# Kernel tuning notes

Hardware: AMD Instinct MI355X
Metric: run time of the kernel (lower is better)

## Reference

```python
import jax, jax.numpy as jnp
import numpy as np

B, T, C, H, KV, D = 2, 2048, 1024, 16, 4, 64
VE_GATE_CH = 32


def _rope(x, cos, sin):
    # x: (B,T,h,D); cos/sin: (1,T,1,D//2); half-split rotary
    d = x.shape[-1] // 2
    x1, x2 = x[..., :d], x[..., d:]
    return jnp.concatenate([x1 * cos + x2 * sin, -x1 * sin + x2 * cos], axis=-1)


def _rms_norm(x, eps=1.1920929e-07):
    # F.rms_norm with no weight; eps defaults to finfo(fp32).eps
    return x * jax.lax.rsqrt(jnp.mean(x * x, axis=-1, keepdims=True) + eps)


def setup_inputs() -> dict:
    key = jax.random.key(0)
    ks = jax.random.split(key, 8)
    x = jax.random.normal(ks[0], (B, T, C), dtype=jnp.float32)
    ve = jax.random.normal(ks[1], (B, T, KV * D), dtype=jnp.float32)
    # standard RoPE tables, half-dim = D//2
    inv_freq = 1.0 / (10000.0 ** (np.arange(0, D, 2, dtype=np.float32) / D))  # (32,)
    freqs = np.arange(T, dtype=np.float32)[:, None] * inv_freq[None, :]       # (T,32)
    cos = jnp.asarray(np.cos(freqs))[None, :, None, :]
    sin = jnp.asarray(np.sin(freqs))[None, :, None, :]
    s = 0.02
    Wq = jax.random.normal(ks[2], (C, H * D), dtype=jnp.float32) * s
    Wk = jax.random.normal(ks[3], (C, KV * D), dtype=jnp.float32) * s
    Wv = jax.random.normal(ks[4], (C, KV * D), dtype=jnp.float32) * s
    Wo = jax.random.normal(ks[5], (C, C), dtype=jnp.float32) * s
    Wg = jax.random.normal(ks[6], (VE_GATE_CH, KV), dtype=jnp.float32) * s
    return {"x": x, "ve": ve, "cos": cos, "sin": sin,
            "Wq": Wq, "Wk": Wk, "Wv": Wv, "Wo": Wo, "Wg": Wg,
            "window": 1024}


def reference(x, ve, cos, sin, Wq, Wk, Wv, Wo, Wg, window):
    b, t, c = x.shape
    q = (x @ Wq).reshape(b, t, H, D)
    k = (x @ Wk).reshape(b, t, KV, D)
    v = (x @ Wv).reshape(b, t, KV, D)
    # value-embedding gating: gate = 2*sigmoid(x[..., :32] @ Wg)
    gate = 2.0 * jax.nn.sigmoid(x[..., :VE_GATE_CH] @ Wg)  # (B,T,KV)
    v = v + gate[..., None] * ve.reshape(b, t, KV, D)
    q = _rms_norm(_rope(q, cos, sin))
    k = _rms_norm(_rope(k, cos, sin))
    # GQA: repeat_interleave kv heads to match query heads
    groups = H // KV
    k = jnp.repeat(k, groups, axis=2)  # (B,T,H,D)
    v = jnp.repeat(v, groups, axis=2)
    scale = 1.0 / jnp.sqrt(jnp.asarray(D, dtype=q.dtype))
    scores = jnp.einsum("bthd,bshd->bhts", q, k) * scale  # (B,H,T,T)
    rows = jnp.arange(t)[:, None]
    cols = jnp.arange(t)[None, :]
    mask = (cols <= rows) & (cols > rows - window)  # causal sliding window
    scores = jnp.where(mask[None, None], scores, jnp.finfo(scores.dtype).min)
    attn = jax.nn.softmax(scores, axis=-1)
    y = jnp.einsum("bhts,bshd->bthd", attn, v).reshape(b, t, c)
    return y @ Wo
```

## Files before the change

### kernel.cpp

```cpp
#include <hip/hip_runtime.h>
#include <hip/hip_bf16.h>

#define B_ 2
#define T_ 2048
#define C_ 1024
#define H_ 16
#define KV_ 4
#define D_ 64
#define M_ (B_*T_)

typedef __attribute__((ext_vector_type(4))) float f32x4;
typedef __attribute__((ext_vector_type(8))) short bf16x8;

__device__ __forceinline__ float exp2fast(float x) {
  return __builtin_amdgcn_exp2f(x);
}

__device__ __forceinline__ unsigned short f2bfu(float f) {
  unsigned u = __builtin_bit_cast(unsigned, f);
  u += 0x7FFFu + ((u >> 16) & 1u);
  return (unsigned short)(u >> 16);
}

__device__ __forceinline__ short f2bf(float f) {
  return (short)f2bfu(f);
}

__device__ __forceinline__ float bf2f(short s) {
  unsigned u = ((unsigned)(unsigned short)s) << 16;
  return __builtin_bit_cast(float, u);
}

__device__ __forceinline__ unsigned cvtpk(float a, float b) {
  unsigned r;
  asm("v_cvt_pk_bf16_f32 %0, %1, %2" : "=v"(r) : "v"(a), "v"(b));
  return r;
}

__device__ __forceinline__ void gld_lds16(const void* g, void* l) {
  __builtin_amdgcn_global_load_lds(
      (const __attribute__((address_space(1))) void*)g,
      (__attribute__((address_space(3))) void*)l, 16, 0, 0);
}

__global__ __launch_bounds__(256) void k_prep(const float* __restrict__ xin,
                                              short* __restrict__ xb,
                                              const float* __restrict__ Wq,
                                              const float* __restrict__ Wk,
                                              const float* __restrict__ Wv,
                                              const float* __restrict__ Wo,
                                              short* __restrict__ wT,
                                              short* __restrict__ woT) {
  __shared__ float tile[32][33];
  const int bid = blockIdx.x;
  const int tid = threadIdx.x;
  if (bid < 4096) {
    int i = (bid * 256 + tid) * 4;
    float4 f = *(const float4*)(xin + i);
    short4 s;
    s.x = f2bf(f.x); s.y = f2bf(f.y); s.z = f2bf(f.z); s.w = f2bf(f.w);
    *(short4*)(xb + i) = s;
    return;
  }
  const int tb = bid - 4096;
  const int bx = tb % 80;
  const int by = tb / 80;
  const int tx = tid & 31, ty = tid >> 5;
  const float* in; short* out; int Ncol, cb;
  if (bx < 32)      { in = Wq; out = wT;                       Ncol = 1024; cb = bx; }
  else if (bx < 40) { in = Wk; out = wT + (size_t)1024 * 1024; Ncol = 256;  cb = bx - 32; }
  else if (bx < 48) { in = Wv; out = wT + (size_t)1280 * 1024; Ncol = 256;  cb = bx - 40; }
  else              { in = Wo; out = woT;                      Ncol = 1024; cb = bx - 48; }
  const int R = 1024;
  int c0 = cb * 32, r0 = by * 32;
#pragma unroll
  for (int i = 0; i < 32; i += 8)
    tile[ty + i][tx] = in[(size_t)(r0 + ty + i) * Ncol + c0 + tx];
  __syncthreads();
#pragma unroll
  for (int i = 0; i < 32; i += 8)
    out[(size_t)(c0 + ty + i) * R + r0 + tx] = f2bf(tile[tx][ty + i]);
}

__global__ __launch_bounds__(256) void k_gemm64(const short* __restrict__ A,
                                                const short* __restrict__ Bt,
                                                float* __restrict__ C,
                                                int M, int N, int K) {
  __shared__ short sA[64 * 64];
  __shared__ short sB[128 * 64];
  const int tid = threadIdx.x;
  const int wid = tid >> 6, lane = tid & 63;
  const int g = lane >> 4, c = lane & 15;
  const int wm = wid >> 1, wn = wid & 1;
  const int m0 = blockIdx.y * 64, n0 = blockIdx.x * 128;
  const int strow = tid >> 3;
  const int scol  = ((tid & 7) ^ (strow & 7)) * 8;
  const int sw = c & 7;

  const short* Ag = A + (size_t)(m0 + strow) * K + scol;
  const short* Bg = Bt + (size_t)(n0 + strow) * K + scol;
  const int ldbase = wid * 512;

  f32x4 acc[2][4] = {};

  for (int k0 = 0; k0 < K; k0 += 64) {
#pragma unroll
    for (int i = 0; i < 2; ++i)
      gld_lds16(Ag + (size_t)(i * 32) * K + k0, &sA[i * 2048 + ldbase]);
#pragma unroll
    for (int i = 0; i < 4; ++i)
      gld_lds16(Bg + (size_t)(i * 32) * K + k0, &sB[i * 2048 + ldbase]);
    __syncthreads();
#pragma unroll
    for (int kk = 0; kk < 2; ++kk) {
      bf16x8 af[2], bfr[4];
#pragma unroll
      for (int i = 0; i < 2; ++i)
        af[i] = *(const bf16x8*)&sA[(wm * 32 + i * 16 + c) * 64 + ((kk * 4 + g) ^ sw) * 8];
#pragma unroll
      for (int j = 0; j < 4; ++j)
        bfr[j] = *(const bf16x8*)&sB[(wn * 64 + j * 16 + c) * 64 + ((kk * 4 + g) ^ sw) * 8];
#pragma unroll
      for (int i = 0; i < 2; ++i)
#pragma unroll
        for (int j = 0; j < 4; ++j)
          acc[i][j] = __builtin_amdgcn_mfma_f32_16x16x32_bf16(af[i], bfr[j], acc[i][j], 0, 0, 0);
    }
    __syncthreads();
  }
#pragma unroll
  for (int i = 0; i < 2; ++i)
#pragma unroll
    for (int j = 0; j < 4; ++j) {
      int row = m0 + wm * 32 + i * 16 + g * 4;
      int col = n0 + wn * 64 + j * 16 + c;
      float* cp = C + (size_t)row * N + col;
#pragma unroll
      for (int r = 0; r < 4; ++r) cp[(size_t)r * N] = acc[i][j][r];
    }
}

__global__ __launch_bounds__(256) void k_gemm_qkv(const short* __restrict__ A,
                                                  const short* __restrict__ Bt,
                                                  short* __restrict__ qkvb,
                                                  short* __restrict__ qb,
                                                  short* __restrict__ kbb,
                                                  const float* __restrict__ cosp,
                                                  const float* __restrict__ sinp) {
  __shared__ short sA[64 * 64];
  __shared__ short sB[128 * 64];
  const int N = 1536, K = 1024;
  const int tid = threadIdx.x;
  const int wid = tid >> 6, lane = tid & 63;
  const int g = lane >> 4, c = lane & 15;
  const int wm = wid >> 1, wn = wid & 1;
  const int m0 = blockIdx.y * 64, n0 = blockIdx.x * 128;
  const int strow = tid >> 3;
  const int scol  = ((tid & 7) ^ (strow & 7)) * 8;
  const int sw = c & 7;

  const short* Ag = A + (size_t)(m0 + strow) * K + scol;
  const short* Bg = Bt + (size_t)(n0 + strow) * K + scol;
  const int ldbase = wid * 512;

  f32x4 acc[2][4] = {};

  for (int k0 = 0; k0 < K; k0 += 64) {
#pragma unroll
    for (int i = 0; i < 2; ++i)
      gld_lds16(Ag + (size_t)(i * 32) * K + k0, &sA[i * 2048 + ldbase]);
#pragma unroll
    for (int i = 0; i < 4; ++i)
      gld_lds16(Bg + (size_t)(i * 32) * K + k0, &sB[i * 2048 + ldbase]);
    __syncthreads();
#pragma unroll
    for (int kk = 0; kk < 2; ++kk) {
      bf16x8 af[2], bfr[4];
#pragma unroll
      for (int i = 0; i < 2; ++i)
        af[i] = *(const bf16x8*)&sA[(wm * 32 + i * 16 + c) * 64 + ((kk * 4 + g) ^ sw) * 8];
#pragma unroll
      for (int j = 0; j < 4; ++j)
        bfr[j] = *(const bf16x8*)&sB[(wn * 64 + j * 16 + c) * 64 + ((kk * 4 + g) ^ sw) * 8];
#pragma unroll
      for (int i = 0; i < 2; ++i)
#pragma unroll
        for (int j = 0; j < 4; ++j)
          acc[i][j] = __builtin_amdgcn_mfma_f32_16x16x32_bf16(af[i], bfr[j], acc[i][j], 0, 0, 0);
    }
    __syncthreads();
  }

  const int head = blockIdx.x * 2 + wn;
  const int b = m0 >> 11;
  const int tbase = (m0 & (T_ - 1)) + wm * 32;
  if (head < 20) {
    short* outbase = (head < 16)
        ? qb  + ((size_t)(b * H_ + head) * T_) * D_
        : kbb + ((size_t)(b * KV_ + (head - 16)) * T_) * D_;
#pragma unroll
    for (int i = 0; i < 2; ++i)
#pragma unroll
      for (int r = 0; r < 4; ++r) {
        const int t = tbase + i * 16 + g * 4 + r;
        const float ca = cosp[t * 32 + c],      sa = sinp[t * 32 + c];
        const float cbv = cosp[t * 32 + 16 + c], sbv = sinp[t * 32 + 16 + c];
        const float f0 = acc[i][0][r], f1 = acc[i][1][r];
        const float f2 = acc[i][2][r], f3 = acc[i][3][r];
        const float r0 = f0 * ca + f2 * sa;
        const float r1 = f1 * cbv + f3 * sbv;
        const float r2 = f2 * ca - f0 * sa;
        const float r3 = f3 * cbv - f1 * sbv;
        float ss = (r0 * r0 + r1 * r1) + (r2 * r2 + r3 * r3);
        ss += __shfl_xor(ss, 1);
        ss += __shfl_xor(ss, 2);
        ss += __shfl_xor(ss, 4);
        ss += __shfl_xor(ss, 8);
        const float sc = rsqrtf(ss * (1.0f / 64.0f) + 1.1920929e-07f);
        unsigned w0 = cvtpk(r0 * sc, r1 * sc);
        unsigned w1 = cvtpk(r2 * sc, r3 * sc);
        unsigned long long w = ((unsigned long long)w1 << 32) | w0;
        *(unsigned long long*)(outbase + (size_t)t * D_ + c * 4) = w;
      }
  } else {
#pragma unroll
    for (int i = 0; i < 2; ++i)
#pragma unroll
      for (int j = 0; j < 4; ++j) {
        int row = m0 + wm * 32 + i * 16 + g * 4;
        int col = n0 + wn * 64 + j * 16 + c;
        short* cp = qkvb + (size_t)row * N + col;
#pragma unroll
        for (int r = 0; r < 4; ++r) cp[(size_t)r * N] = f2bf(acc[i][j][r]);
      }
  }
}

__global__ __launch_bounds__(256) void k_vtrans(const short* __restrict__ qkvb,
                                                const float* __restrict__ ve,
                                                const float* __restrict__ x,
                                                const float* __restrict__ Wg,
                                                short* __restrict__ vT) {
  const int t0 = blockIdx.x * 64;
  const int bk = blockIdx.y;
  const int b = bk >> 2, kv = bk & 3;
  const int tx = threadIdx.x;
  const int ty = threadIdx.y;
  __shared__ float tile[64][65];
  __shared__ float sgate[64];
  if (ty == 0) {
    const int row = b * T_ + t0 + tx;
    const float* xr = x + (size_t)row * C_;
    float a = 0.0f;
#pragma unroll 8
    for (int kk = 0; kk < 32; ++kk) a = fmaf(xr[kk], Wg[kk * KV_ + kv], a);
    sgate[tx] = 2.0f / (1.0f + __expf(-a));
  }
  __syncthreads();
#pragma unroll
  for (int i = 0; i < 16; ++i) {
    const int tr = ty + 4 * i;
    const int row = b * T_ + t0 + tr;
    float gt = sgate[tr];
    float v = bf2f(qkvb[(size_t)row * 1536 + 1280 + kv * 64 + tx]);
    v = fmaf(gt, ve[(size_t)row * (KV_ * D_) + kv * 64 + tx], v);
    tile[tr][tx] = v;
  }
  __syncthreads();
#pragma unroll
  for (int i = 0; i < 16; ++i) {
    const int d = ty + 4 * i;
    vT[((size_t)bk * 64 + d) * T_ + t0 + tx] = f2bf(tile[tx][d]);
  }
}

__global__ __launch_bounds__(512, 6) void k_attn(const short* __restrict__ qg,
                                                 const short* __restrict__ kg,
                                                 const short* __restrict__ vg,
                                                 short* __restrict__ yb,
                                                 const int* __restrict__ winp) {
  const int wsz = *winp;
  const int qt = blockIdx.x, bh = blockIdx.y;
  const int b = bh >> 4, h = bh & 15;
  const int kvh = h >> 2;
  const int tid = threadIdx.x;
  const int wid = tid >> 6, lane = tid & 63;
  const int g = lane >> 4, c = lane & 15;
  const int t0 = qt * 128 + wid * 16;

  __shared__ short sK[2][64 * 64];
  __shared__ short sV[2][64 * 64];
  __shared__ short spt_all[8][16][72];
  short (*spt)[72] = spt_all[wid];

  const short* qbase = qg + ((size_t)(b * H_ + h) * T_ + t0) * D_;
  const bf16x8 bq0 = *(const bf16x8*)(qbase + c * D_ + g * 8);
  const bf16x8 bq1 = *(const bf16x8*)(qbase + c * D_ + 32 + g * 8);
  const short* kbase = kg + (size_t)(b * KV_ + kvh) * T_ * D_;
  const short* vbase = vg + (size_t)(b * KV_ + kvh) * D_ * T_;

  const int srow0 = tid >> 3;
  const int sq    = ((tid & 7) ^ (srow0 & 7)) * 8;
  const int ldst0 = wid * 512;

  float m = -20000.0f, l = 0.0f;
  f32x4 o[4] = {};

  int lo = t0 - wsz + 1; if (lo < 0) lo = 0;
  const int kt_lo_w = lo >> 6;
  const int kt_hi_w = (t0 + 15) >> 6;
  int lou = qt * 128 - wsz + 1; if (lou < 0) lou = 0;
  const int kt_lo_u = lou >> 6;
  const int kt_hi_u = 2 * qt + 1;
  const int qgl = t0 + c;
  const float SC2 = 0.125f * 1.44269504088896340736f;

  {
    const short* ksrc = kbase + (size_t)(kt_lo_u * 64 + srow0) * D_ + sq;
    gld_lds16(ksrc, &sK[0][ldst0]);
    const short* vsrc = vbase + (size_t)srow0 * T_ + kt_lo_u * 64 + sq;
    gld_lds16(vsrc, &sV[0][ldst0]);
  }
  __syncthreads();

  int cb = 0;
  for (int kt = kt_lo_u; kt <= kt_hi_u; ++kt) {
    const int kc0 = kt * 64;
    if (kt < kt_hi_u) {
      const short* ksrc = kbase + (size_t)((kt + 1) * 64 + srow0) * D_ + sq;
      gld_lds16(ksrc, &sK[cb ^ 1][ldst0]);
      const short* vsrc = vbase + (size_t)srow0 * T_ + (kt + 1) * 64 + sq;
      gld_lds16(vsrc, &sV[cb ^ 1][ldst0]);
    }
    if (kt >= kt_lo_w && kt <= kt_hi_w) {
      f32x4 s[4] = {};
#pragma unroll
      for (int cj = 0; cj < 4; ++cj) {
        const int rbase = (cj * 16 + c) * 64;
        const int sw = (c & 7);
        bf16x8 k0 = *(const bf16x8*)&sK[cb][rbase + ((g ^ sw) * 8)];
        bf16x8 k1 = *(const bf16x8*)&sK[cb][rbase + (((4 + g) ^ sw) * 8)];
        s[cj] = __builtin_amdgcn_mfma_f32_16x16x32_bf16(k0, bq0, s[cj], 0, 0, 0);
        s[cj] = __builtin_amdgcn_mfma_f32_16x16x32_bf16(k1, bq1, s[cj], 0, 0, 0);
      }
      const bool edge = (kt >= kt_hi_w) || (kt <= kt_lo_w + 1);
      float tmax = -3.0e38f;
#pragma unroll
      for (int cj = 0; cj < 4; ++cj)
#pragma unroll
        for (int r = 0; r < 4; ++r) {
          float v = s[cj][r];
          if (edge) {
            int kv = kc0 + cj * 16 + 4 * g + r;
            v = (kv <= qgl && kv > qgl - wsz) ? v : -1.0e9f;
            s[cj][r] = v;
          }
          tmax = fmaxf(tmax, v);
        }
      tmax = fmaxf(tmax, __shfl_xor(tmax, 16));
      tmax = fmaxf(tmax, __shfl_xor(tmax, 32));
      const float tms = tmax * SC2;
      if (!__all(tms <= m + 8.0f)) {
        const float nm = fmaxf(m, tms);
        const float fr = exp2fast(m - nm);
        m = nm;
        l *= fr;
#pragma unroll
        for (int nd = 0; nd < 4; ++nd)
#pragma unroll
          for (int r = 0; r < 4; ++r) o[nd][r] *= fr;
      }
      const float negm = -m;
      float psum = 0.0f;
      unsigned pb[8];
#pragma unroll
      for (int cj = 0; cj < 4; ++cj) {
        float p0 = exp2fast(fmaf(s[cj][0], SC2, negm));
        float p1 = exp2fast(fmaf(s[cj][1], SC2, negm));
        float p2 = exp2fast(fmaf(s[cj][2], SC2, negm));
        float p3 = exp2fast(fmaf(s[cj][3], SC2, negm));
        psum += (p0 + p1) + (p2 + p3);
        pb[2 * cj]     = cvtpk(p0, p1);
        pb[2 * cj + 1] = cvtpk(p2, p3);
      }
      psum += __shfl_xor(psum, 16);
      psum += __shfl_xor(psum, 32);
      l += psum;
#pragma unroll
      for (int cj = 0; cj < 4; ++cj) {
        unsigned long long w = ((unsigned long long)pb[2 * cj + 1] << 32) | pb[2 * cj];
        *(unsigned long long*)&spt[c][cj * 16 + 4 * g] = w;
      }
      asm volatile("s_waitcnt lgkmcnt(0)" ::: "memory");
#pragma unroll
      for (int ks = 0; ks < 2; ++ks) {
        bf16x8 bp = *(const bf16x8*)&spt[c][ks * 32 + g * 8];
#pragma unroll
        for (int nd = 0; nd < 4; ++nd) {
          const int rbase = (nd * 16 + c) * 64;
          bf16x8 bv = *(const bf16x8*)&sV[cb][rbase + (((ks * 4 + g) ^ (c & 7)) * 8)];
          o[nd] = __builtin_amdgcn_mfma_f32_16x16x32_bf16(bv, bp, o[nd], 0, 0, 0);
        }
      }
    }
    __syncthreads();
    cb ^= 1;
  }
  const float inv = 1.0f / l;
#pragma unroll
  for (int nd = 0; nd < 4; ++nd) {
    unsigned d0 = cvtpk(o[nd][0] * inv, o[nd][1] * inv);
    unsigned d1 = cvtpk(o[nd][2] * inv, o[nd][3] * inv);
    unsigned long long w = ((unsigned long long)d1 << 32) | d0;
    *(unsigned long long*)(yb + ((size_t)b * T_ + t0 + c) * C_ + h * D_ + nd * 16 + 4 * g) = w;
  }
}

extern "C" void kernel_launch(void* const* d_in, const int* in_sizes, int n_in,
                              void* d_out, int out_size, void* d_ws, size_t ws_size,
                              hipStream_t stream) {
  const float* x    = (const float*)d_in[0];
  const float* ve   = (const float*)d_in[1];
  const float* cosp = (const float*)d_in[2];
  const float* sinp = (const float*)d_in[3];
  const float* Wq   = (const float*)d_in[4];
  const float* Wk   = (const float*)d_in[5];
  const float* Wv   = (const float*)d_in[6];
  const float* Wo   = (const float*)d_in[7];
  const float* Wg   = (const float*)d_in[8];
  const int*   winp = (const int*)d_in[9];
  float* out = (float*)d_out;
  char* ws = (char*)d_ws;

  const size_t MB = 1024 * 1024;
  short* xb    = (short*)(ws);
  short* wT    = (short*)(ws + 8  * MB);
  short* woT   = (short*)(ws + 11 * MB);
  short* qkvb  = (short*)(ws + 13 * MB);
  short* qb    = (short*)(ws + 25 * MB);
  short* kbuf  = (short*)(ws + 33 * MB);
  short* vT    = (short*)(ws + 35 * MB);
  short* yb    = (short*)(ws + 37 * MB);

  k_prep<<<6656, 256, 0, stream>>>(x, xb, Wq, Wk, Wv, Wo, wT, woT);
  k_gemm_qkv<<<dim3(12, 64), 256, 0, stream>>>(xb, wT, qkvb, qb, kbuf, cosp, sinp);
  k_vtrans<<<dim3(32, 8), dim3(64, 4), 0, stream>>>(qkvb, ve, x, Wg, vT);
  k_attn<<<dim3(16, 32), 512, 0, stream>>>(qb, kbuf, vT, yb, winp);
  k_gemm64<<<dim3(8, 64), 256, 0, stream>>>(yb, woT, out, M_, 1024, 1024);
}
```

Baseline: 92.67 us.

## Single-buffer V tile, halve P staging buffer, defer row-sum reduction in attention

The attention kernel drops double-buffering of the V tile. V is now loaded into a single LDS buffer at the start of each iteration and overlaps with the QK^T and softmax work, with an extra barrier before PV. The per-warp P staging buffer shrinks to half width and is written and read in two passes, and the cross-lane reduction of the softmax denominator moves out of the loop to the end. The goal is lower LDS use and fewer per-iteration shuffles, possibly allowing more resident blocks, at the cost of an extra __syncthreads per tile, less prefetch lead for V, and dropping the occupancy hint in launch bounds.

After: 92.41 us (median of 2 runs). No clear change (-0.3%).

```diff
diff --git a/kernel.cpp b/kernel.cpp
--- a/kernel.cpp
+++ b/kernel.cpp
@@ -274,11 +274,11 @@
   }
 }
 
-__global__ __launch_bounds__(512, 6) void k_attn(const short* __restrict__ qg,
-                                                 const short* __restrict__ kg,
-                                                 const short* __restrict__ vg,
-                                                 short* __restrict__ yb,
-                                                 const int* __restrict__ winp) {
+__global__ __launch_bounds__(512) void k_attn(const short* __restrict__ qg,
+                                              const short* __restrict__ kg,
+                                              const short* __restrict__ vg,
+                                              short* __restrict__ yb,
+                                              const int* __restrict__ winp) {
   const int wsz = *winp;
   const int qt = blockIdx.x, bh = blockIdx.y;
   const int b = bh >> 4, h = bh & 15;
@@ -289,9 +289,9 @@
   const int t0 = qt * 128 + wid * 16;
 
   __shared__ short sK[2][64 * 64];
-  __shared__ short sV[2][64 * 64];
-  __shared__ short spt_all[8][16][72];
-  short (*spt)[72] = spt_all[wid];
+  __shared__ short sV[64 * 64];
+  __shared__ short spt_all[8][16][40];
+  short (*spt)[40] = spt_all[wid];
 
   const short* qbase = qg + ((size_t)(b * H_ + h) * T_ + t0) * D_;
   const bf16x8 bq0 = *(const bf16x8*)(qbase + c * D_ + g * 8);
@@ -318,21 +318,25 @@
   {
     const short* ksrc = kbase + (size_t)(kt_lo_u * 64 + srow0) * D_ + sq;
     gld_lds16(ksrc, &sK[0][ldst0]);
-    const short* vsrc = vbase + (size_t)srow0 * T_ + kt_lo_u * 64 + sq;
-    gld_lds16(vsrc, &sV[0][ldst0]);
   }
   __syncthreads();
 
   int cb = 0;
   for (int kt = kt_lo_u; kt <= kt_hi_u; ++kt) {
     const int kc0 = kt * 64;
+    {
+      const short* vsrc = vbase + (size_t)srow0 * T_ + kc0 + sq;
+      gld_lds16(vsrc, &sV[ldst0]);
+    }
     if (kt < kt_hi_u) {
       const short* ksrc = kbase + (size_t)((kt + 1) * 64 + srow0) * D_ + sq;
       gld_lds16(ksrc, &sK[cb ^ 1][ldst0]);
-      const short* vsrc = vbase + (size_t)srow0 * T_ + (kt + 1) * 64 + sq;
-      gld_lds16(vsrc, &sV[cb ^ 1][ldst0]);
-    }
-    if (kt >= kt_lo_w && kt <= kt_hi_w) {
+    }
+    const bool active = (kt >= kt_lo_w && kt <= kt_hi_w);
+    unsigned pb[8];
+    float fr = 1.0f;
+    bool doresc = false;
+    if (active) {
       f32x4 s[4] = {};
 #pragma unroll
       for (int cj = 0; cj < 4; ++cj) {
@@ -360,19 +364,15 @@
       tmax = fmaxf(tmax, __shfl_xor(tmax, 16));
       tmax = fmaxf(tmax, __shfl_xor(tmax, 32));
       const float tms = tmax * SC2;
-      if (!__all(tms <= m + 8.0f)) {
+      doresc = !__all(tms <= m + 8.0f);
+      if (doresc) {
         const float nm = fmaxf(m, tms);
-        const float fr = exp2fast(m - nm);
+        fr = exp2fast(m - nm);
         m = nm;
         l *= fr;
-#pragma unroll
-        for (int nd = 0; nd < 4; ++nd)
-#pragma unroll
-          for (int r = 0; r < 4; ++r) o[nd][r] *= fr;
       }
       const float negm = -m;
       float psum = 0.0f;
-      unsigned pb[8];
 #pragma unroll
       for (int cj = 0; cj < 4; ++cj) {
         float p0 = exp2fast(fmaf(s[cj][0], SC2, negm));
@@ -383,29 +383,51 @@
         pb[2 * cj]     = cvtpk(p0, p1);
         pb[2 * cj + 1] = cvtpk(p2, p3);
       }
-      psum += __shfl_xor(psum, 16);
-      psum += __shfl_xor(psum, 32);
       l += psum;
-#pragma unroll
-      for (int cj = 0; cj < 4; ++cj) {
-        unsigned long long w = ((unsigned long long)pb[2 * cj + 1] << 32) | pb[2 * cj];
-        *(unsigned long long*)&spt[c][cj * 16 + 4 * g] = w;
+    }
+    __syncthreads();
+    if (active) {
+      {
+        unsigned long long w0 = ((unsigned long long)pb[1] << 32) | pb[0];
+        unsigned long long w1 = ((unsigned long long)pb[3] << 32) | pb[2];
+        *(unsigned long long*)&spt[c][4 * g]      = w0;
+        *(unsigned long long*)&spt[c][16 + 4 * g] = w1;
+      }
+      if (doresc) {
+#pragma unroll
+        for (int nd = 0; nd < 4; ++nd)
+#pragma unroll
+          for (int r = 0; r < 4; ++r) o[nd][r] *= fr;
       }
       asm volatile("s_waitcnt lgkmcnt(0)" ::: "memory");
-#pragma unroll
-      for (int ks = 0; ks < 2; ++ks) {
-        bf16x8 bp = *(const bf16x8*)&spt[c][ks * 32 + g * 8];
-#pragma unroll
-        for (int nd = 0; nd < 4; ++nd) {
-          const int rbase = (nd * 16 + c) * 64;
-          bf16x8 bv = *(const bf16x8*)&sV[cb][rbase + (((ks * 4 + g) ^ (c & 7)) * 8)];
-          o[nd] = __builtin_amdgcn_mfma_f32_16x16x32_bf16(bv, bp, o[nd], 0, 0, 0);
-        }
+      bf16x8 bp0 = *(const bf16x8*)&spt[c][8 * g];
+#pragma unroll
+      for (int nd = 0; nd < 4; ++nd) {
+        const int rbase = (nd * 16 + c) * 64;
+        bf16x8 bv = *(const bf16x8*)&sV[rbase + ((g ^ (c & 7)) * 8)];
+        o[nd] = __builtin_amdgcn_mfma_f32_16x16x32_bf16(bv, bp0, o[nd], 0, 0, 0);
+      }
+      asm volatile("s_waitcnt lgkmcnt(0)" ::: "memory");
+      {
+        unsigned long long w0 = ((unsigned long long)pb[5] << 32) | pb[4];
+        unsigned long long w1 = ((unsigned long long)pb[7] << 32) | pb[6];
+        *(unsigned long long*)&spt[c][4 * g]      = w0;
+        *(unsigned long long*)&spt[c][16 + 4 * g] = w1;
+      }
+      asm volatile("s_waitcnt lgkmcnt(0)" ::: "memory");
+      bf16x8 bp1 = *(const bf16x8*)&spt[c][8 * g];
+#pragma unroll
+      for (int nd = 0; nd < 4; ++nd) {
+        const int rbase = (nd * 16 + c) * 64;
+        bf16x8 bv = *(const bf16x8*)&sV[rbase + (((4 + g) ^ (c & 7)) * 8)];
+        o[nd] = __builtin_amdgcn_mfma_f32_16x16x32_bf16(bv, bp1, o[nd], 0, 0, 0);
       }
     }
     __syncthreads();
     cb ^= 1;
   }
+  l += __shfl_xor(l, 16);
+  l += __shfl_xor(l, 32);
   const float inv = 1.0f / l;
 #pragma unroll
   for (int nd = 0; nd < 4; ++nd) {
```
